# Kernel optimization log

Hardware: AMD Instinct MI355X
Metric: run time of the kernel (lower is better)

Reference implementation:

```python
import jax, jax.numpy as jnp
import numpy as np

EPS = 1e-6

# config matching the torch module: ctx != 'object_ord', bp == 'sgmn', tracker=False, opt='add'

def setup_inputs() -> dict:
    bs, nseq, num_box, num_ctx, max_len = 32, 24, 196, 196, 6
    key = jax.random.key(0)
    ks = jax.random.split(key, 8)
    ent_attn = jax.random.normal(ks[0], (bs, nseq, num_box), dtype=jnp.float32)
    spo_attn = jax.random.normal(ks[1], (bs, nseq, num_box, num_ctx), dtype=jnp.float32)
    ctx_idx_adjusted = jax.random.randint(ks[2], (bs, num_box, num_ctx), 0, num_box, dtype=jnp.int32)
    cls_raw = jax.random.randint(ks[3], (bs, num_box), 0, 100, dtype=jnp.int32)
    roi_cls = jnp.where(cls_raw < 90, cls_raw, -1)
    roi_mask = (jax.random.uniform(ks[4], (bs, num_box, num_ctx)) < 0.9).astype(jnp.float32)
    weight_on_children = jax.random.uniform(ks[5], (bs, nseq, num_box), dtype=jnp.float32)
    traversal_lists = jax.random.randint(ks[6], (bs, max_len), 0, nseq, dtype=jnp.int32)
    adj_raw = jax.random.randint(ks[7], (bs, nseq, nseq), 0, 2 * nseq, dtype=jnp.int32)
    adj_matrices = jnp.where(adj_raw < nseq, adj_raw, -1)
    return {
        'traversal_lists': traversal_lists,
        'adj_matrices': adj_matrices,
        'ent_attn': ent_attn,
        'spo_attn': spo_attn,
        'ctx_idx_adjusted': ctx_idx_adjusted,
        'roi_cls': roi_cls,
        'roi_mask': roi_mask,
        'weight_on_children': weight_on_children,
    }


def _bottom_up(traversal_lists, adj_matrices, ent_attn, spo_attn,
               ctx_idx_adjusted, roi_cls, roi_mask, weight_on_children):
    bs, nseq, num_box = ent_attn.shape
    k_cls = (roi_cls != -1).astype(ent_attn.dtype)           # [bs, num_box]
    batch_ix = jnp.arange(bs)
    # per-batch gather: child_atn[b, j, ctx[b, i, c]]
    gather_ctx = jax.vmap(lambda ca, ci: ca[:, ci])           # ([nseq,nb],[nb,nc]) -> [nseq,nb,nc]

    def step(ea, p):  # p: [bs] parent ids for this traversal step
        valid_p = p >= 0
        pc = jnp.maximum(p, 0)
        # edge ids from parent row of adjacency: [bs, nseq]
        edges = jnp.take_along_axis(adj_matrices, pc[:, None, None], axis=1)[:, 0]
        cmask = (edges >= 0) & valid_p[:, None]               # which columns are real children
        cm = cmask.astype(ea.dtype)
        ec = jnp.maximum(edges, 0)
        # children attention, zeroed for non-children and invalid ROI classes
        child_atn = ea * cm[:, :, None] * k_cls[:, None, :]   # [bs, nseq, num_box]
        # gather "child could be context c of box i" scores
        gathered = gather_ctx(child_atn, ctx_idx_adjusted)    # [bs, nseq, num_box, num_ctx]
        fmask = roi_mask[:, None] * cm[:, :, None, None]      # filter_mask per child row
        sc = gathered * fmask                                 # k_scores_children_be_any_ctx
        rel = jnp.take_along_axis(spo_attn, ec[:, :, None, None], axis=1)
        sr = rel * fmask * k_cls[:, None, :, None]            # k_scores_rel_by_any_edge
        # sgmn transfer: sum over ctx dim (extra roi_mask multiply as in torch)
        core = jnp.sum(sc * sr * roi_mask[:, None], axis=-1)  # [bs, nseq, num_box]
        nch = jnp.sum(cm, axis=1)                             # [bs]
        neff = jnp.maximum(nch, 1.0)                          # dummy child when no children
        add_to_sub = jnp.sum(core, axis=1) + neff[:, None] * EPS  # opt='add' -> sum over children
        sub_atn = jnp.take_along_axis(ea, pc[:, None, None], axis=1)[:, 0]        # [bs, num_box]
        w = jnp.take_along_axis(weight_on_children, pc[:, None, None], axis=1)[:, 0]
        upd = sub_atn + add_to_sub * w
        # NormAttnMap('cossim'): divide by detached max |.| clipped at 1
        norm = jax.lax.stop_gradient(jnp.max(jnp.abs(upd), axis=-1, keepdims=True))
        norm = jnp.where(norm <= 1.0, 1.0, norm)
        upd = upd / norm
        upd = jnp.where(roi_cls == -1, -1.0, upd)             # opt='add' branch sets -1
        write = valid_p & (nch > 0)                           # bs_mask
        new_row = jnp.where(write[:, None], upd, sub_atn)
        ea = ea.at[batch_ix, pc].set(new_row)
        return ea, None

    ea, _ = jax.lax.scan(step, ent_attn, traversal_lists.T)
    return ea


def reference(traversal_lists, adj_matrices, ent_attn, spo_attn,
              ctx_idx_adjusted, roi_cls, roi_mask, weight_on_children):
    return _bottom_up(traversal_lists, adj_matrices, ent_attn, spo_attn,
                      ctx_idx_adjusted, roi_cls, roi_mask, weight_on_children)
```

## Files before the change

### kernel.cpp

```cpp
#include <hip/hip_runtime.h>

#define NSEQ   24
#define NBOX   196
#define NCTX   196
#define MAXLEN 6
#define EPSV   1e-6f
#define BS     32

#define TILES      25
#define K1T        512
#define NB4        49
#define ROWP       200

#define MIDX_ELEMS ((size_t)BS * NBOX * NCTX)

__global__ __launch_bounds__(K1T, 6) void step_compute(
    const float* __restrict__ src,
    float*       __restrict__ ea_copy,
    const float* __restrict__ spo,
    const int*   __restrict__ ctx,
    const int*   __restrict__ roi_cls,
    const float* __restrict__ rm,
    const int*   __restrict__ trav,
    const int*   __restrict__ adj,
    int*         __restrict__ midx,
    float*       __restrict__ araw,
    int step, int mode)
{
    const int b    = blockIdx.x / TILES;
    const int tile = blockIdx.x % TILES;
    const int tid  = threadIdx.x;
    const int wave = tid >> 6;
    const int lane = tid & 63;

    __shared__ __align__(16) float cae[NSEQ][ROWP];

    if (step == 0) {
        const int total4 = BS * NSEQ * NBOX / 4;
        int idx = blockIdx.x * K1T + tid;
        if (idx < total4) ((float4*)ea_copy)[idx] = ((const float4*)src)[idx];
    }

    const int p = trav[b * MAXLEN + step];
    int e = -1;
    if (p >= 0 && lane < NSEQ)
        e = adj[((size_t)b * NSEQ + p) * NSEQ + lane];
    const unsigned long long mask = __ballot(e >= 0);
    const int nch = __popcll(mask);

    int ec = 0, jc = 0;
    if (nch > 0) {
        unsigned long long m = mask;
        const int lim = (lane < NSEQ) ? lane : NSEQ;
        for (int k = 0; k < lim; ++k) m &= (m - 1);
        const int j0 = __ffsll(mask) - 1;
        const int jn = m ? (__ffsll(m) - 1) : j0;
        jc = (lane < nch) ? jn : j0;
        ec = __shfl(e, jc);
    }

    if (nch > 0) {
        for (int n = wave; n < nch; n += 8) {
            const int j = __shfl(jc, n);
            if (lane < 50) {
                float4 v = make_float4(0.f, 0.f, 0.f, 0.f);
                if (lane < NB4) {
                    float4 e4 = ((const float4*)(src + ((size_t)b * NSEQ + j) * NBOX))[lane];
                    int4   r4 = ((const int4*)(roi_cls + b * NBOX))[lane];
                    v.x = (r4.x != -1) ? e4.x : 0.f;
                    v.y = (r4.y != -1) ? e4.y : 0.f;
                    v.z = (r4.z != -1) ? e4.z : 0.f;
                    v.w = (r4.w != -1) ? e4.w : 0.f;
                }
                ((float4*)&cae[n][0])[lane] = v;
            }
        }
        __syncthreads();
    }

    const int i = tile * 8 + wave;
    if (i >= NBOX) return;

    float acc = 0.f;
    if (lane < NB4) {
        const size_t bi = (size_t)b * NBOX + i;
        int4 mi;
        if (mode == 2) {
            mi = ((const int4*)(midx + bi * NCTX))[lane];
        } else {
            const int4   ix = ((const int4*)  (ctx + bi * NCTX))[lane];
            const float4 m4 = ((const float4*)(rm  + bi * NCTX))[lane];
            mi.x = (m4.x != 0.f) ? ix.x : NBOX;
            mi.y = (m4.y != 0.f) ? ix.y : NBOX;
            mi.z = (m4.z != 0.f) ? ix.z : NBOX;
            mi.w = (m4.w != 0.f) ? ix.w : NBOX;
            if (mode == 1) ((int4*)(midx + bi * NCTX))[lane] = mi;
        }

        if (nch > 0) {
            const float* sb = spo + ((size_t)b * NSEQ * NBOX + i) * NCTX;
            const size_t st = (size_t)NBOX * NCTX;
            const int e0 = __shfl(ec, 0), e1 = __shfl(ec, 1), e2 = __shfl(ec, 2);
            float4 s0 = ((const float4*)(sb + (size_t)e0 * st))[lane];
            float4 s1 = ((const float4*)(sb + (size_t)e1 * st))[lane];
            float4 s2 = ((const float4*)(sb + (size_t)e2 * st))[lane];
            float4 a4 = make_float4(0.f, 0.f, 0.f, 0.f);
            for (int n = 0; n < nch; ++n) {
                const int ep = __shfl(ec, n + 3);
                float4 nx = ((const float4*)(sb + (size_t)ep * st))[lane];
                a4.x = fmaf(cae[n][mi.x], s0.x, a4.x);
                a4.y = fmaf(cae[n][mi.y], s0.y, a4.y);
                a4.z = fmaf(cae[n][mi.z], s0.z, a4.z);
                a4.w = fmaf(cae[n][mi.w], s0.w, a4.w);
                s0 = s1; s1 = s2; s2 = nx;
            }
            acc = (a4.x + a4.y) + (a4.z + a4.w);
        }
    }

    if (nch > 0) {
        #pragma unroll
        for (int off = 32; off >= 1; off >>= 1)
            acc += __shfl_down(acc, off, 64);
        if (lane == 0) {
            float kci = (roi_cls[b * NBOX + i] != -1) ? 1.0f : 0.0f;
            araw[b * NBOX + i] = kci * acc;
        }
    }
}

__global__ __launch_bounds__(256) void step_finalize(
    float*       __restrict__ ea,
    const float* __restrict__ araw,
    const float* __restrict__ wc,
    const int*   __restrict__ roi_cls,
    const int*   __restrict__ trav,
    const int*   __restrict__ adj,
    int step)
{
    const int b   = blockIdx.x;
    const int tid = threadIdx.x;
    const int p   = trav[b * MAXLEN + step];

    int nch = 0;
    if (p >= 0) {
        const int* arow = adj + ((size_t)b * NSEQ + p) * NSEQ;
        for (int j = 0; j < NSEQ; ++j) nch += (arow[j] >= 0) ? 1 : 0;
    }
    if (p < 0 || nch == 0) return;

    float upd = 0.0f, a = 0.0f;
    if (tid < NBOX) {
        const float sub = ea[((size_t)b * NSEQ + p) * NBOX + tid];
        const float w   = wc[((size_t)b * NSEQ + p) * NBOX + tid];
        upd = sub + (araw[b * NBOX + tid] + (float)nch * EPSV) * w;
        a = fabsf(upd);
    }
    #pragma unroll
    for (int off = 32; off >= 1; off >>= 1)
        a = fmaxf(a, __shfl_down(a, off, 64));
    __shared__ float wmax[4];
    if ((tid & 63) == 0) wmax[tid >> 6] = a;
    __syncthreads();
    float norm = fmaxf(fmaxf(wmax[0], wmax[1]), fmaxf(wmax[2], wmax[3]));
    norm = (norm <= 1.0f) ? 1.0f : norm;
    if (tid < NBOX) {
        float val = upd / norm;
        if (roi_cls[b * NBOX + tid] == -1) val = -1.0f;
        ea[((size_t)b * NSEQ + p) * NBOX + tid] = val;
    }
}

extern "C" void kernel_launch(void* const* d_in, const int* in_sizes, int n_in,
                              void* d_out, int out_size, void* d_ws, size_t ws_size,
                              hipStream_t stream) {
    const int*   trav = (const int*)  d_in[0];
    const int*   adj  = (const int*)  d_in[1];
    const float* ent  = (const float*)d_in[2];
    const float* spo  = (const float*)d_in[3];
    const int*   ctx  = (const int*)  d_in[4];
    const int*   roi  = (const int*)  d_in[5];
    const float* rm   = (const float*)d_in[6];
    const float* wc   = (const float*)d_in[7];

    float* ea = (float*)d_out;

    const bool ws_ok = ws_size >= (MIDX_ELEMS + (size_t)BS * NBOX) * 4;
    int*   midx = (int*)d_ws;
    float* araw = ws_ok ? ((float*)d_ws + MIDX_ELEMS) : (float*)d_ws;

    for (int t = 0; t < MAXLEN; ++t) {
        const int mode = ws_ok ? (t == 0 ? 1 : 2) : 0;
        step_compute<<<BS * TILES, K1T, 0, stream>>>(
            t == 0 ? ent : ea, ea, spo, ctx, roi, rm, trav, adj,
            midx, araw, t, mode);
        step_finalize<<<BS, 256, 0, stream>>>(
            ea, araw, wc, roi, trav, adj, t);
    }
}
```

Measured before the change: 101.2 us.

## Transpose child-attention shared tile with XOR swizzle and batch four children per load

The per-batch child attention rows are stored in shared memory transposed to [box][child], padded to 32 children and XOR-swizzled. A single float4 LDS at a gathered context index now returns four children's values, and the inner loop handles children in groups of four, issuing four spo row loads per group. This cuts the number of random-index LDS operations and exposes more independent global loads. In exchange, every block must zero the whole shared tile, and padded children read valid but unused spo rows. The kernel also returns early when a parent has no children, which skips the step-0 midx write for that batch.

Measured after the change: 102.9 us. No clear change (+1.6%).

```diff
diff --git a/kernel.cpp b/kernel.cpp
--- a/kernel.cpp
+++ b/kernel.cpp
@@ -7,10 +7,11 @@
 #define EPSV   1e-6f
 #define BS     32
 
-#define TILES      25
-#define K1T        512
-#define NB4        49
-#define ROWP       200
+#define TILES  25
+#define K1T    512
+#define NB4    49
+#define CROW   32
+#define CROWS  200
 
 #define MIDX_ELEMS ((size_t)BS * NBOX * NCTX)
 
@@ -33,12 +34,19 @@
     const int wave = tid >> 6;
     const int lane = tid & 63;
 
-    __shared__ __align__(16) float cae[NSEQ][ROWP];
+    __shared__ __align__(16) float caeT[CROWS * CROW];
+    __shared__ int s_childJ[NSEQ];
 
     if (step == 0) {
         const int total4 = BS * NSEQ * NBOX / 4;
         int idx = blockIdx.x * K1T + tid;
         if (idx < total4) ((float4*)ea_copy)[idx] = ((const float4*)src)[idx];
+    }
+
+    {
+        const float4 z = make_float4(0.f, 0.f, 0.f, 0.f);
+        for (int t = tid; t < CROWS * CROW / 4; t += K1T)
+            ((float4*)caeT)[t] = z;
     }
 
     const int p = trav[b * MAXLEN + step];
@@ -47,9 +55,10 @@
         e = adj[((size_t)b * NSEQ + p) * NSEQ + lane];
     const unsigned long long mask = __ballot(e >= 0);
     const int nch = __popcll(mask);
-
-    int ec = 0, jc = 0;
-    if (nch > 0) {
+    if (nch == 0) return;
+
+    int ec, jc;
+    {
         unsigned long long m = mask;
         const int lim = (lane < NSEQ) ? lane : NSEQ;
         for (int k = 0; k < lim; ++k) m &= (m - 1);
@@ -57,26 +66,19 @@
         const int jn = m ? (__ffsll(m) - 1) : j0;
         jc = (lane < nch) ? jn : j0;
         ec = __shfl(e, jc);
-    }
-
-    if (nch > 0) {
-        for (int n = wave; n < nch; n += 8) {
-            const int j = __shfl(jc, n);
-            if (lane < 50) {
-                float4 v = make_float4(0.f, 0.f, 0.f, 0.f);
-                if (lane < NB4) {
-                    float4 e4 = ((const float4*)(src + ((size_t)b * NSEQ + j) * NBOX))[lane];
-                    int4   r4 = ((const int4*)(roi_cls + b * NBOX))[lane];
-                    v.x = (r4.x != -1) ? e4.x : 0.f;
-                    v.y = (r4.y != -1) ? e4.y : 0.f;
-                    v.z = (r4.z != -1) ? e4.z : 0.f;
-                    v.w = (r4.w != -1) ? e4.w : 0.f;
-                }
-                ((float4*)&cae[n][0])[lane] = v;
-            }
-        }
-        __syncthreads();
-    }
+        if (wave == 0 && lane < nch) s_childJ[lane] = jc;
+    }
+    __syncthreads();
+
+    for (int t = tid; t < nch * NBOX; t += K1T) {
+        const int n = t / NBOX;
+        const int k = t - n * NBOX;
+        const int j = s_childJ[n];
+        float v = src[((size_t)b * NSEQ + j) * NBOX + k];
+        v = (roi_cls[b * NBOX + k] != -1) ? v : 0.f;
+        caeT[k * CROW + 4 * ((n >> 2) ^ (k & 7)) + (n & 3)] = v;
+    }
+    __syncthreads();
 
     const int i = tile * 8 + wave;
     if (i >= NBOX) return;
@@ -96,36 +98,48 @@
             mi.w = (m4.w != 0.f) ? ix.w : NBOX;
             if (mode == 1) ((int4*)(midx + bi * NCTX))[lane] = mi;
         }
-
-        if (nch > 0) {
-            const float* sb = spo + ((size_t)b * NSEQ * NBOX + i) * NCTX;
-            const size_t st = (size_t)NBOX * NCTX;
-            const int e0 = __shfl(ec, 0), e1 = __shfl(ec, 1), e2 = __shfl(ec, 2);
-            float4 s0 = ((const float4*)(sb + (size_t)e0 * st))[lane];
-            float4 s1 = ((const float4*)(sb + (size_t)e1 * st))[lane];
-            float4 s2 = ((const float4*)(sb + (size_t)e2 * st))[lane];
-            float4 a4 = make_float4(0.f, 0.f, 0.f, 0.f);
-            for (int n = 0; n < nch; ++n) {
-                const int ep = __shfl(ec, n + 3);
-                float4 nx = ((const float4*)(sb + (size_t)ep * st))[lane];
-                a4.x = fmaf(cae[n][mi.x], s0.x, a4.x);
-                a4.y = fmaf(cae[n][mi.y], s0.y, a4.y);
-                a4.z = fmaf(cae[n][mi.z], s0.z, a4.z);
-                a4.w = fmaf(cae[n][mi.w], s0.w, a4.w);
-                s0 = s1; s1 = s2; s2 = nx;
-            }
-            acc = (a4.x + a4.y) + (a4.z + a4.w);
+        const int rbx = mi.x * CROW, c7x = mi.x & 7;
+        const int rby = mi.y * CROW, c7y = mi.y & 7;
+        const int rbz = mi.z * CROW, c7z = mi.z & 7;
+        const int rbw = mi.w * CROW, c7w = mi.w & 7;
+
+        const float* sb = spo + ((size_t)b * NSEQ * NBOX + i) * NCTX;
+        const size_t st = (size_t)NBOX * NCTX;
+        const int nq = (nch + 3) >> 2;
+
+        float4 a4 = make_float4(0.f, 0.f, 0.f, 0.f);
+        for (int nb = 0; nb < nq; ++nb) {
+            const int n4 = nb << 2;
+            const int e0 = __shfl(ec, n4);
+            const int e1 = __shfl(ec, n4 + 1);
+            const int e2 = __shfl(ec, n4 + 2);
+            const int e3 = __shfl(ec, n4 + 3);
+            const float4 s0 = ((const float4*)(sb + (size_t)e0 * st))[lane];
+            const float4 s1 = ((const float4*)(sb + (size_t)e1 * st))[lane];
+            const float4 s2 = ((const float4*)(sb + (size_t)e2 * st))[lane];
+            const float4 s3 = ((const float4*)(sb + (size_t)e3 * st))[lane];
+            const float4 cx = *(const float4*)&caeT[rbx + ((nb ^ c7x) << 2)];
+            const float4 cy = *(const float4*)&caeT[rby + ((nb ^ c7y) << 2)];
+            const float4 cz = *(const float4*)&caeT[rbz + ((nb ^ c7z) << 2)];
+            const float4 cw = *(const float4*)&caeT[rbw + ((nb ^ c7w) << 2)];
+            a4.x = fmaf(cx.x, s0.x, a4.x); a4.x = fmaf(cx.y, s1.x, a4.x);
+            a4.x = fmaf(cx.z, s2.x, a4.x); a4.x = fmaf(cx.w, s3.x, a4.x);
+            a4.y = fmaf(cy.x, s0.y, a4.y); a4.y = fmaf(cy.y, s1.y, a4.y);
+            a4.y = fmaf(cy.z, s2.y, a4.y); a4.y = fmaf(cy.w, s3.y, a4.y);
+            a4.z = fmaf(cz.x, s0.z, a4.z); a4.z = fmaf(cz.y, s1.z, a4.z);
+            a4.z = fmaf(cz.z, s2.z, a4.z); a4.z = fmaf(cz.w, s3.z, a4.z);
+            a4.w = fmaf(cw.x, s0.w, a4.w); a4.w = fmaf(cw.y, s1.w, a4.w);
+            a4.w = fmaf(cw.z, s2.w, a4.w); a4.w = fmaf(cw.w, s3.w, a4.w);
         }
-    }
-
-    if (nch > 0) {
-        #pragma unroll
-        for (int off = 32; off >= 1; off >>= 1)
-            acc += __shfl_down(acc, off, 64);
-        if (lane == 0) {
-            float kci = (roi_cls[b * NBOX + i] != -1) ? 1.0f : 0.0f;
-            araw[b * NBOX + i] = kci * acc;
-        }
+        acc = (a4.x + a4.y) + (a4.z + a4.w);
+    }
+
+    #pragma unroll
+    for (int off = 32; off >= 1; off >>= 1)
+        acc += __shfl_down(acc, off, 64);
+    if (lane == 0) {
+        float kci = (roi_cls[b * NBOX + i] != -1) ? 1.0f : 0.0f;
+        araw[b * NBOX + i] = kci * acc;
     }
 }
 
```

## Fuse all traversal steps into one persistent kernel with per-batch spin barriers

Applied to the files above, without the earlier changes.

The twelve per-step compute and finalize launches become a single persistent kernel. Each batch gets 16 blocks, and those blocks synchronize across steps through atomic counters in workspace. The finalize of the previous step is folded redundantly into every block at the start of the next step, and the freshly normalized row is forwarded through shared memory to avoid a global round trip. This removes launch overhead and inter-kernel gaps, at the cost of spin-wait barriers that assume all blocks are co-resident, plus a small zeroing kernel.

Measured after the change: 274.8 us. 171% more time.

```diff
diff --git a/kernel.cpp b/kernel.cpp
--- a/kernel.cpp
+++ b/kernel.cpp
@@ -6,168 +6,213 @@
 #define MAXLEN 6
 #define EPSV   1e-6f
 #define BS     32
-
-#define TILES      25
-#define K1T        512
-#define NB4        49
-#define ROWP       200
+#define BPB    16
+#define GRID   (BS * BPB)
+#define THR    512
+#define NB4    49
+#define ROWP   200
 
 #define MIDX_ELEMS ((size_t)BS * NBOX * NCTX)
-
-__global__ __launch_bounds__(K1T, 6) void step_compute(
-    const float* __restrict__ src,
-    float*       __restrict__ ea_copy,
+#define CNT_N      (MAXLEN * BS * 16)
+
+__global__ void zero_cnt(unsigned* __restrict__ cnt) {
+    int i = blockIdx.x * blockDim.x + threadIdx.x;
+    if (i < CNT_N) cnt[i] = 0u;
+}
+
+__device__ __forceinline__ float blockmax(float a, float* s_red, int tid) {
+    #pragma unroll
+    for (int off = 32; off >= 1; off >>= 1)
+        a = fmaxf(a, __shfl_down(a, off, 64));
+    if ((tid & 63) == 0) s_red[tid >> 6] = a;
+    __syncthreads();
+    return fmaxf(fmaxf(fmaxf(s_red[0], s_red[1]), fmaxf(s_red[2], s_red[3])),
+                 fmaxf(fmaxf(s_red[4], s_red[5]), fmaxf(s_red[6], s_red[7])));
+}
+
+__global__ __launch_bounds__(THR, 4) void bottom_up(
+    const float* __restrict__ ent,
+    float*       __restrict__ ea,
     const float* __restrict__ spo,
     const int*   __restrict__ ctx,
     const int*   __restrict__ roi_cls,
     const float* __restrict__ rm,
+    const float* __restrict__ wc,
     const int*   __restrict__ trav,
     const int*   __restrict__ adj,
     int*         __restrict__ midx,
     float*       __restrict__ araw,
-    int step, int mode)
+    float*       __restrict__ oldrow,
+    unsigned*    __restrict__ cnt)
 {
-    const int b    = blockIdx.x / TILES;
-    const int tile = blockIdx.x % TILES;
+    const int blk  = blockIdx.x;
+    const int b    = blk >> 4;
+    const int sub  = blk & 15;
     const int tid  = threadIdx.x;
     const int wave = tid >> 6;
     const int lane = tid & 63;
 
     __shared__ __align__(16) float cae[NSEQ][ROWP];
-
-    if (step == 0) {
-        const int total4 = BS * NSEQ * NBOX / 4;
-        int idx = blockIdx.x * K1T + tid;
-        if (idx < total4) ((float4*)ea_copy)[idx] = ((const float4*)src)[idx];
-    }
-
-    const int p = trav[b * MAXLEN + step];
-    int e = -1;
-    if (p >= 0 && lane < NSEQ)
-        e = adj[((size_t)b * NSEQ + p) * NSEQ + lane];
-    const unsigned long long mask = __ballot(e >= 0);
-    const int nch = __popcll(mask);
-
-    int ec = 0, jc = 0;
-    if (nch > 0) {
-        unsigned long long m = mask;
-        const int lim = (lane < NSEQ) ? lane : NSEQ;
-        for (int k = 0; k < lim; ++k) m &= (m - 1);
-        const int j0 = __ffsll(mask) - 1;
-        const int jn = m ? (__ffsll(m) - 1) : j0;
-        jc = (lane < nch) ? jn : j0;
-        ec = __shfl(e, jc);
-    }
-
-    if (nch > 0) {
-        for (int n = wave; n < nch; n += 8) {
-            const int j = __shfl(jc, n);
-            if (lane < 50) {
-                float4 v = make_float4(0.f, 0.f, 0.f, 0.f);
-                if (lane < NB4) {
-                    float4 e4 = ((const float4*)(src + ((size_t)b * NSEQ + j) * NBOX))[lane];
-                    int4   r4 = ((const int4*)(roi_cls + b * NBOX))[lane];
-                    v.x = (r4.x != -1) ? e4.x : 0.f;
-                    v.y = (r4.y != -1) ? e4.y : 0.f;
-                    v.z = (r4.z != -1) ? e4.z : 0.f;
-                    v.w = (r4.w != -1) ? e4.w : 0.f;
-                }
-                ((float4*)&cae[n][0])[lane] = v;
-            }
-        }
-        __syncthreads();
-    }
-
-    const int i = tile * 8 + wave;
-    if (i >= NBOX) return;
-
-    float acc = 0.f;
-    if (lane < NB4) {
-        const size_t bi = (size_t)b * NBOX + i;
-        int4 mi;
-        if (mode == 2) {
-            mi = ((const int4*)(midx + bi * NCTX))[lane];
-        } else {
+    __shared__ float s_fin[NBOX];
+    __shared__ float s_red[8];
+    __shared__ int   s_childJ[NSEQ];
+
+    if (tid < NSEQ * 4) cae[tid >> 2][NBOX + (tid & 3)] = 0.f;
+
+    {
+        const int idx = sub * THR + tid;
+        if (idx < NSEQ * NBOX / 4)
+            ((float4*)(ea + (size_t)b * NSEQ * NBOX))[idx] =
+                ((const float4*)(ent + (size_t)b * NSEQ * NBOX))[idx];
+    }
+
+    for (int k = wave; ; k += 8) {
+        const int i = sub + 16 * k;
+        if (i >= NBOX) break;
+        if (lane < NB4) {
+            const size_t bi = (size_t)b * NBOX + i;
             const int4   ix = ((const int4*)  (ctx + bi * NCTX))[lane];
             const float4 m4 = ((const float4*)(rm  + bi * NCTX))[lane];
+            int4 mi;
             mi.x = (m4.x != 0.f) ? ix.x : NBOX;
             mi.y = (m4.y != 0.f) ? ix.y : NBOX;
             mi.z = (m4.z != 0.f) ? ix.z : NBOX;
             mi.w = (m4.w != 0.f) ? ix.w : NBOX;
-            if (mode == 1) ((int4*)(midx + bi * NCTX))[lane] = mi;
-        }
-
+            ((int4*)(midx + bi * NCTX))[lane] = mi;
+        }
+    }
+
+    int p_prev = -1, nch_prev = 0;
+
+    for (int t = 0; t < MAXLEN; ++t) {
+        const float* src = (t == 0) ? ent : ea;
+        const bool prevvalid = (p_prev >= 0 && nch_prev > 0);
+
+        const int p = trav[b * MAXLEN + t];
+        int e = -1;
+        if (p >= 0 && lane < NSEQ)
+            e = adj[((size_t)b * NSEQ + p) * NSEQ + lane];
+        const unsigned long long mask = __ballot(e >= 0);
+        const int nch = __popcll(mask);
+        int ec = 0;
         if (nch > 0) {
-            const float* sb = spo + ((size_t)b * NSEQ * NBOX + i) * NCTX;
-            const size_t st = (size_t)NBOX * NCTX;
-            const int e0 = __shfl(ec, 0), e1 = __shfl(ec, 1), e2 = __shfl(ec, 2);
-            float4 s0 = ((const float4*)(sb + (size_t)e0 * st))[lane];
-            float4 s1 = ((const float4*)(sb + (size_t)e1 * st))[lane];
-            float4 s2 = ((const float4*)(sb + (size_t)e2 * st))[lane];
-            float4 a4 = make_float4(0.f, 0.f, 0.f, 0.f);
-            for (int n = 0; n < nch; ++n) {
-                const int ep = __shfl(ec, n + 3);
-                float4 nx = ((const float4*)(sb + (size_t)ep * st))[lane];
-                a4.x = fmaf(cae[n][mi.x], s0.x, a4.x);
-                a4.y = fmaf(cae[n][mi.y], s0.y, a4.y);
-                a4.z = fmaf(cae[n][mi.z], s0.z, a4.z);
-                a4.w = fmaf(cae[n][mi.w], s0.w, a4.w);
-                s0 = s1; s1 = s2; s2 = nx;
-            }
-            acc = (a4.x + a4.y) + (a4.z + a4.w);
-        }
-    }
-
-    if (nch > 0) {
-        #pragma unroll
-        for (int off = 32; off >= 1; off >>= 1)
-            acc += __shfl_down(acc, off, 64);
-        if (lane == 0) {
-            float kci = (roi_cls[b * NBOX + i] != -1) ? 1.0f : 0.0f;
-            araw[b * NBOX + i] = kci * acc;
-        }
-    }
-}
-
-__global__ __launch_bounds__(256) void step_finalize(
-    float*       __restrict__ ea,
-    const float* __restrict__ araw,
-    const float* __restrict__ wc,
-    const int*   __restrict__ roi_cls,
-    const int*   __restrict__ trav,
-    const int*   __restrict__ adj,
-    int step)
-{
-    const int b   = blockIdx.x;
-    const int tid = threadIdx.x;
-    const int p   = trav[b * MAXLEN + step];
-
-    int nch = 0;
-    if (p >= 0) {
-        const int* arow = adj + ((size_t)b * NSEQ + p) * NSEQ;
-        for (int j = 0; j < NSEQ; ++j) nch += (arow[j] >= 0) ? 1 : 0;
-    }
-    if (p < 0 || nch == 0) return;
-
-    float upd = 0.0f, a = 0.0f;
-    if (tid < NBOX) {
-        const float sub = ea[((size_t)b * NSEQ + p) * NBOX + tid];
-        const float w   = wc[((size_t)b * NSEQ + p) * NBOX + tid];
-        upd = sub + (araw[b * NBOX + tid] + (float)nch * EPSV) * w;
-        a = fabsf(upd);
-    }
-    #pragma unroll
-    for (int off = 32; off >= 1; off >>= 1)
-        a = fmaxf(a, __shfl_down(a, off, 64));
-    __shared__ float wmax[4];
-    if ((tid & 63) == 0) wmax[tid >> 6] = a;
-    __syncthreads();
-    float norm = fmaxf(fmaxf(wmax[0], wmax[1]), fmaxf(wmax[2], wmax[3]));
-    norm = (norm <= 1.0f) ? 1.0f : norm;
-    if (tid < NBOX) {
-        float val = upd / norm;
-        if (roi_cls[b * NBOX + tid] == -1) val = -1.0f;
-        ea[((size_t)b * NSEQ + p) * NBOX + tid] = val;
+            unsigned long long m = mask;
+            const int lim = (lane < NSEQ) ? lane : NSEQ;
+            for (int k = 0; k < lim; ++k) m &= (m - 1);
+            const int j0 = __ffsll(mask) - 1;
+            const int jn = m ? (__ffsll(m) - 1) : j0;
+            const int jc = (lane < nch) ? jn : j0;
+            ec = __shfl(e, jc);
+            if (wave == 0 && lane < nch) s_childJ[lane] = jc;
+        }
+
+        if (prevvalid) {
+            float u = 0.f, a = 0.f;
+            if (tid < NBOX) {
+                const float old = oldrow[(size_t)((t - 1) & 1) * BS * NBOX + b * NBOX + tid];
+                const float w   = wc[((size_t)b * NSEQ + p_prev) * NBOX + tid];
+                u = old + (araw[(size_t)(t - 1) * BS * NBOX + b * NBOX + tid]
+                           + (float)nch_prev * EPSV) * w;
+                a = fabsf(u);
+            }
+            float norm = blockmax(a, s_red, tid);
+            norm = (norm <= 1.0f) ? 1.0f : norm;
+            if (tid < NBOX) {
+                float v = u / norm;
+                if (roi_cls[b * NBOX + tid] == -1) v = -1.0f;
+                s_fin[tid] = v;
+                if (sub == 0)
+                    ea[((size_t)b * NSEQ + p_prev) * NBOX + tid] = v;
+            }
+            __syncthreads();
+        }
+
+        if (p >= 0 && sub == 0 && tid < NBOX) {
+            float sv = (prevvalid && p == p_prev)
+                       ? s_fin[tid]
+                       : src[((size_t)b * NSEQ + p) * NBOX + tid];
+            oldrow[(size_t)(t & 1) * BS * NBOX + b * NBOX + tid] = sv;
+        }
+
+        if (nch > 0) {
+            __syncthreads();
+
+            for (int t2 = tid; t2 < nch * NBOX; t2 += THR) {
+                const int n = t2 / NBOX;
+                const int k = t2 - n * NBOX;
+                const int j = s_childJ[n];
+                float v = (prevvalid && j == p_prev)
+                          ? s_fin[k]
+                          : src[((size_t)b * NSEQ + j) * NBOX + k];
+                cae[n][k] = (roi_cls[b * NBOX + k] != -1) ? v : 0.f;
+            }
+            __syncthreads();
+
+            for (int k = wave; ; k += 8) {
+                const int i = sub + 16 * k;
+                if (i >= NBOX) break;
+                float acc = 0.f;
+                if (lane < NB4) {
+                    const size_t bi = (size_t)b * NBOX + i;
+                    const int4 mi = ((const int4*)(midx + bi * NCTX))[lane];
+                    const float* sb = spo + ((size_t)b * NSEQ * NBOX + i) * NCTX;
+                    const size_t st = (size_t)NBOX * NCTX;
+                    const int e0 = __shfl(ec, 0), e1 = __shfl(ec, 1), e2 = __shfl(ec, 2);
+                    float4 s0 = ((const float4*)(sb + (size_t)e0 * st))[lane];
+                    float4 s1 = ((const float4*)(sb + (size_t)e1 * st))[lane];
+                    float4 s2 = ((const float4*)(sb + (size_t)e2 * st))[lane];
+                    float4 a4 = make_float4(0.f, 0.f, 0.f, 0.f);
+                    for (int n = 0; n < nch; ++n) {
+                        const int ep = __shfl(ec, (n + 3 < nch) ? n + 3 : 0);
+                        float4 nx = ((const float4*)(sb + (size_t)ep * st))[lane];
+                        a4.x = fmaf(cae[n][mi.x], s0.x, a4.x);
+                        a4.y = fmaf(cae[n][mi.y], s0.y, a4.y);
+                        a4.z = fmaf(cae[n][mi.z], s0.z, a4.z);
+                        a4.w = fmaf(cae[n][mi.w], s0.w, a4.w);
+                        s0 = s1; s1 = s2; s2 = nx;
+                    }
+                    acc = (a4.x + a4.y) + (a4.z + a4.w);
+                }
+                #pragma unroll
+                for (int off = 32; off >= 1; off >>= 1)
+                    acc += __shfl_down(acc, off, 64);
+                if (lane == 0) {
+                    float kci = (roi_cls[b * NBOX + i] != -1) ? 1.0f : 0.0f;
+                    araw[(size_t)t * BS * NBOX + b * NBOX + i] = kci * acc;
+                }
+            }
+        }
+
+        __syncthreads();
+        if (tid == 0) {
+            __threadfence();
+            unsigned* c = &cnt[(t * BS + b) * 16];
+            atomicAdd(c, 1u);
+            while (atomicAdd(c, 0u) < (unsigned)BPB)
+                __builtin_amdgcn_s_sleep(2);
+            __threadfence();
+        }
+        __syncthreads();
+
+        p_prev = p; nch_prev = nch;
+    }
+
+    if (sub == 0 && p_prev >= 0 && nch_prev > 0) {
+        float u = 0.f, a = 0.f;
+        if (tid < NBOX) {
+            const float old = oldrow[(size_t)((MAXLEN - 1) & 1) * BS * NBOX + b * NBOX + tid];
+            const float w   = wc[((size_t)b * NSEQ + p_prev) * NBOX + tid];
+            u = old + (araw[(size_t)(MAXLEN - 1) * BS * NBOX + b * NBOX + tid]
+                       + (float)nch_prev * EPSV) * w;
+            a = fabsf(u);
+        }
+        float norm = blockmax(a, s_red, tid);
+        norm = (norm <= 1.0f) ? 1.0f : norm;
+        if (tid < NBOX) {
+            float v = u / norm;
+            if (roi_cls[b * NBOX + tid] == -1) v = -1.0f;
+            ea[((size_t)b * NSEQ + p_prev) * NBOX + tid] = v;
+        }
     }
 }
 
@@ -185,16 +230,13 @@
 
     float* ea = (float*)d_out;
 
-    const bool ws_ok = ws_size >= (MIDX_ELEMS + (size_t)BS * NBOX) * 4;
-    int*   midx = (int*)d_ws;
-    float* araw = ws_ok ? ((float*)d_ws + MIDX_ELEMS) : (float*)d_ws;
-
-    for (int t = 0; t < MAXLEN; ++t) {
-        const int mode = ws_ok ? (t == 0 ? 1 : 2) : 0;
-        step_compute<<<BS * TILES, K1T, 0, stream>>>(
-            t == 0 ? ent : ea, ea, spo, ctx, roi, rm, trav, adj,
-            midx, araw, t, mode);
-        step_finalize<<<BS, 256, 0, stream>>>(
-            ea, araw, wc, roi, trav, adj, t);
-    }
-}
+    size_t off = MIDX_ELEMS;
+    int*      midx   = (int*)d_ws;
+    float*    araw   = (float*)d_ws + off;      off += (size_t)MAXLEN * BS * NBOX;
+    float*    oldrow = (float*)d_ws + off;      off += (size_t)2 * BS * NBOX;
+    unsigned* cnt    = (unsigned*)((float*)d_ws + off);
+
+    zero_cnt<<<(CNT_N + 255) / 256, 256, 0, stream>>>(cnt);
+    bottom_up<<<GRID, THR, 0, stream>>>(
+        ent, ea, spo, ctx, roi, rm, wc, trav, adj, midx, araw, oldrow, cnt);
+}
```

## Fuse finalize into compute via last-block atomic counter and compress midx to bytes

Applied to the files above, without the earlier changes.

Folds the per-step finalize kernel into the compute kernel. Each tile block increments a per-(step,batch) atomic counter, and the last block to arrive does the normalization and write-back. This halves the number of launches and removes the gap between them. The cached masked context index array is stored as uint8 instead of int32, which cuts its memory traffic by four. A small init kernel zeros the counters, adding one launch and relying on threadfence ordering for correctness.

Measured after the change: 232.6 us. 2.3x slower.

```diff
diff --git a/kernel.cpp b/kernel.cpp
--- a/kernel.cpp
+++ b/kernel.cpp
@@ -7,24 +7,32 @@
 #define EPSV   1e-6f
 #define BS     32
 
-#define TILES      25
-#define K1T        512
-#define NB4        49
-#define ROWP       200
-
-#define MIDX_ELEMS ((size_t)BS * NBOX * NCTX)
+#define TILES  25
+#define K1T    512
+#define NB4    49
+#define ROWP   200
+
+#define MIDX_BYTES ((size_t)BS * NBOX * NCTX)
+#define DONE_N     (MAXLEN * BS * 16)
+
+__global__ void init_ws(unsigned* __restrict__ done) {
+    int i = blockIdx.x * blockDim.x + threadIdx.x;
+    if (i < DONE_N) done[i] = 0u;
+}
 
 __global__ __launch_bounds__(K1T, 6) void step_compute(
     const float* __restrict__ src,
-    float*       __restrict__ ea_copy,
+    float*       __restrict__ ea,
     const float* __restrict__ spo,
     const int*   __restrict__ ctx,
     const int*   __restrict__ roi_cls,
     const float* __restrict__ rm,
+    const float* __restrict__ wc,
     const int*   __restrict__ trav,
     const int*   __restrict__ adj,
-    int*         __restrict__ midx,
+    unsigned char* __restrict__ midx,
     float*       __restrict__ araw,
+    unsigned*    __restrict__ done,
     int step, int mode)
 {
     const int b    = blockIdx.x / TILES;
@@ -34,11 +42,15 @@
     const int lane = tid & 63;
 
     __shared__ __align__(16) float cae[NSEQ][ROWP];
+    __shared__ float s_red[8];
+    __shared__ int   s_childJ[NSEQ];
+    __shared__ int   s_flag;
 
     if (step == 0) {
-        const int total4 = BS * NSEQ * NBOX / 4;
-        int idx = blockIdx.x * K1T + tid;
-        if (idx < total4) ((float4*)ea_copy)[idx] = ((const float4*)src)[idx];
+        const int idx = tile * K1T + tid;
+        if (idx < NSEQ * NBOX / 4)
+            ((float4*)(ea + (size_t)b * NSEQ * NBOX))[idx] =
+                ((const float4*)(src + (size_t)b * NSEQ * NBOX))[idx];
     }
 
     const int p = trav[b * MAXLEN + step];
@@ -47,46 +59,25 @@
         e = adj[((size_t)b * NSEQ + p) * NSEQ + lane];
     const unsigned long long mask = __ballot(e >= 0);
     const int nch = __popcll(mask);
-
-    int ec = 0, jc = 0;
+    int ec = 0;
     if (nch > 0) {
         unsigned long long m = mask;
         const int lim = (lane < NSEQ) ? lane : NSEQ;
         for (int k = 0; k < lim; ++k) m &= (m - 1);
         const int j0 = __ffsll(mask) - 1;
         const int jn = m ? (__ffsll(m) - 1) : j0;
-        jc = (lane < nch) ? jn : j0;
+        const int jc = (lane < nch) ? jn : j0;
         ec = __shfl(e, jc);
-    }
-
-    if (nch > 0) {
-        for (int n = wave; n < nch; n += 8) {
-            const int j = __shfl(jc, n);
-            if (lane < 50) {
-                float4 v = make_float4(0.f, 0.f, 0.f, 0.f);
-                if (lane < NB4) {
-                    float4 e4 = ((const float4*)(src + ((size_t)b * NSEQ + j) * NBOX))[lane];
-                    int4   r4 = ((const int4*)(roi_cls + b * NBOX))[lane];
-                    v.x = (r4.x != -1) ? e4.x : 0.f;
-                    v.y = (r4.y != -1) ? e4.y : 0.f;
-                    v.z = (r4.z != -1) ? e4.z : 0.f;
-                    v.w = (r4.w != -1) ? e4.w : 0.f;
-                }
-                ((float4*)&cae[n][0])[lane] = v;
-            }
-        }
-        __syncthreads();
+        if (wave == 0 && lane < nch) s_childJ[lane] = jc;
     }
 
     const int i = tile * 8 + wave;
-    if (i >= NBOX) return;
-
-    float acc = 0.f;
-    if (lane < NB4) {
+    int4 mi = make_int4(NBOX, NBOX, NBOX, NBOX);
+    if (i < NBOX && lane < NB4) {
         const size_t bi = (size_t)b * NBOX + i;
-        int4 mi;
         if (mode == 2) {
-            mi = ((const int4*)(midx + bi * NCTX))[lane];
+            const uchar4 u = ((const uchar4*)(midx + bi * NCTX))[lane];
+            mi = make_int4(u.x, u.y, u.z, u.w);
         } else {
             const int4   ix = ((const int4*)  (ctx + bi * NCTX))[lane];
             const float4 m4 = ((const float4*)(rm  + bi * NCTX))[lane];
@@ -94,10 +85,37 @@
             mi.y = (m4.y != 0.f) ? ix.y : NBOX;
             mi.z = (m4.z != 0.f) ? ix.z : NBOX;
             mi.w = (m4.w != 0.f) ? ix.w : NBOX;
-            if (mode == 1) ((int4*)(midx + bi * NCTX))[lane] = mi;
-        }
-
-        if (nch > 0) {
+            if (mode == 1)
+                ((uchar4*)(midx + bi * NCTX))[lane] =
+                    make_uchar4((unsigned char)mi.x, (unsigned char)mi.y,
+                                (unsigned char)mi.z, (unsigned char)mi.w);
+        }
+    }
+
+    if (nch == 0) return;
+
+    __syncthreads();
+
+    for (int n = wave; n < nch; n += 8) {
+        const int j = s_childJ[n];
+        if (lane < 50) {
+            float4 v = make_float4(0.f, 0.f, 0.f, 0.f);
+            if (lane < NB4) {
+                const float4 e4 = ((const float4*)(src + ((size_t)b * NSEQ + j) * NBOX))[lane];
+                const int4   r4 = ((const int4*)(roi_cls + b * NBOX))[lane];
+                v.x = (r4.x != -1) ? e4.x : 0.f;
+                v.y = (r4.y != -1) ? e4.y : 0.f;
+                v.z = (r4.z != -1) ? e4.z : 0.f;
+                v.w = (r4.w != -1) ? e4.w : 0.f;
+            }
+            ((float4*)&cae[n][0])[lane] = v;
+        }
+    }
+    __syncthreads();
+
+    if (i < NBOX) {
+        float acc = 0.f;
+        if (lane < NB4) {
             const float* sb = spo + ((size_t)b * NSEQ * NBOX + i) * NCTX;
             const size_t st = (size_t)NBOX * NCTX;
             const int e0 = __shfl(ec, 0), e1 = __shfl(ec, 1), e2 = __shfl(ec, 2);
@@ -116,9 +134,6 @@
             }
             acc = (a4.x + a4.y) + (a4.z + a4.w);
         }
-    }
-
-    if (nch > 0) {
         #pragma unroll
         for (int off = 32; off >= 1; off >>= 1)
             acc += __shfl_down(acc, off, 64);
@@ -127,47 +142,37 @@
             araw[b * NBOX + i] = kci * acc;
         }
     }
-}
-
-__global__ __launch_bounds__(256) void step_finalize(
-    float*       __restrict__ ea,
-    const float* __restrict__ araw,
-    const float* __restrict__ wc,
-    const int*   __restrict__ roi_cls,
-    const int*   __restrict__ trav,
-    const int*   __restrict__ adj,
-    int step)
-{
-    const int b   = blockIdx.x;
-    const int tid = threadIdx.x;
-    const int p   = trav[b * MAXLEN + step];
-
-    int nch = 0;
-    if (p >= 0) {
-        const int* arow = adj + ((size_t)b * NSEQ + p) * NSEQ;
-        for (int j = 0; j < NSEQ; ++j) nch += (arow[j] >= 0) ? 1 : 0;
-    }
-    if (p < 0 || nch == 0) return;
-
-    float upd = 0.0f, a = 0.0f;
+
+    __syncthreads();
+    if (tid == 0) {
+        __threadfence();
+        const unsigned old = atomicAdd(&done[(step * BS + b) * 16], 1u);
+        const int win = (old == TILES - 1);
+        if (win) __threadfence();
+        s_flag = win;
+    }
+    __syncthreads();
+    if (!s_flag) return;
+
+    float u = 0.f, a = 0.f;
     if (tid < NBOX) {
         const float sub = ea[((size_t)b * NSEQ + p) * NBOX + tid];
         const float w   = wc[((size_t)b * NSEQ + p) * NBOX + tid];
-        upd = sub + (araw[b * NBOX + tid] + (float)nch * EPSV) * w;
-        a = fabsf(upd);
+        u = sub + (araw[b * NBOX + tid] + (float)nch * EPSV) * w;
+        a = fabsf(u);
     }
     #pragma unroll
     for (int off = 32; off >= 1; off >>= 1)
         a = fmaxf(a, __shfl_down(a, off, 64));
-    __shared__ float wmax[4];
-    if ((tid & 63) == 0) wmax[tid >> 6] = a;
-    __syncthreads();
-    float norm = fmaxf(fmaxf(wmax[0], wmax[1]), fmaxf(wmax[2], wmax[3]));
+    if ((tid & 63) == 0) s_red[tid >> 6] = a;
+    __syncthreads();
+    float norm = fmaxf(fmaxf(fmaxf(s_red[0], s_red[1]), fmaxf(s_red[2], s_red[3])),
+                       fmaxf(fmaxf(s_red[4], s_red[5]), fmaxf(s_red[6], s_red[7])));
     norm = (norm <= 1.0f) ? 1.0f : norm;
     if (tid < NBOX) {
-        float val = upd / norm;
-        if (roi_cls[b * NBOX + tid] == -1) val = -1.0f;
-        ea[((size_t)b * NSEQ + p) * NBOX + tid] = val;
+        float v = u / norm;
+        if (roi_cls[b * NBOX + tid] == -1) v = -1.0f;
+        ea[((size_t)b * NSEQ + p) * NBOX + tid] = v;
     }
 }
 
@@ -185,16 +190,27 @@
 
     float* ea = (float*)d_out;
 
-    const bool ws_ok = ws_size >= (MIDX_ELEMS + (size_t)BS * NBOX) * 4;
-    int*   midx = (int*)d_ws;
-    float* araw = ws_ok ? ((float*)d_ws + MIDX_ELEMS) : (float*)d_ws;
+    const size_t need = MIDX_BYTES + (size_t)BS * NBOX * 4 + (size_t)DONE_N * 4;
+    const bool ws_ok = ws_size >= need;
+    unsigned char* midx;
+    float*         araw;
+    unsigned*      done;
+    if (ws_ok) {
+        midx = (unsigned char*)d_ws;
+        araw = (float*)((char*)d_ws + MIDX_BYTES);
+        done = (unsigned*)((char*)d_ws + MIDX_BYTES + (size_t)BS * NBOX * 4);
+    } else {
+        midx = (unsigned char*)d_ws;
+        araw = (float*)d_ws;
+        done = (unsigned*)((char*)d_ws + (size_t)BS * NBOX * 4);
+    }
+
+    init_ws<<<(DONE_N + 255) / 256, 256, 0, stream>>>(done);
 
     for (int t = 0; t < MAXLEN; ++t) {
         const int mode = ws_ok ? (t == 0 ? 1 : 2) : 0;
         step_compute<<<BS * TILES, K1T, 0, stream>>>(
-            t == 0 ? ent : ea, ea, spo, ctx, roi, rm, trav, adj,
-            midx, araw, t, mode);
-        step_finalize<<<BS, 256, 0, stream>>>(
-            ea, araw, wc, roi, trav, adj, t);
+            t == 0 ? ent : ea, ea, spo, ctx, roi, rm, wc, trav, adj,
+            midx, araw, done, t, mode);
     }
 }
```
